# Kernel tuning notes

Measured on AMD Instinct MI355X. Metric: run time of the kernel, lower is better.

Reference implementation:

```python
import jax, jax.numpy as jnp
import numpy as np

WS = 8      # window_size
NH = 6      # num_heads
SHIFT = 4   # shift_size


def setup_inputs() -> dict:
    key = jax.random.key(0)
    k0, k1, k2, k3, k4 = jax.random.split(key, 5)
    B, C, H, W = 4, 192, 224, 224
    x = jax.random.normal(k0, (B, C, H, W), jnp.float32)
    # 1x1 convs == per-pixel linear layers: store weights as (out, in)
    w_qkv = jax.random.normal(k1, (3 * C, C), jnp.float32) * 0.05
    b_qkv = jax.random.normal(k2, (3 * C,), jnp.float32) * 0.05
    w_proj = jax.random.normal(k3, (C, C), jnp.float32) * 0.05
    b_proj = jax.random.normal(k4, (C,), jnp.float32) * 0.05
    return {"x": x, "w_qkv": w_qkv, "b_qkv": b_qkv, "w_proj": w_proj, "b_proj": b_proj}


def reference(x, w_qkv, b_qkv, w_proj, b_proj):
    B, C, H, W = x.shape
    hd = C // NH
    scale = hd ** -0.5

    if SHIFT > 0:
        x = jnp.roll(x, shift=(-SHIFT, -SHIFT), axis=(2, 3))

    pad_r = (WS - W % WS) % WS
    pad_b = (WS - H % WS) % WS
    if pad_r > 0 or pad_b > 0:
        x = jnp.pad(x, ((0, 0), (0, 0), (0, pad_b), (0, pad_r)))
    Hp, Wp = x.shape[2], x.shape[3]
    Hn, Wn = Hp // WS, Wp // WS

    # qkv 1x1 conv: (B,C,Hp,Wp) -> (B,3C,Hp,Wp)
    qkv = jnp.einsum('bchw,oc->bohw', x, w_qkv) + b_qkv[None, :, None, None]

    # (B,3,NH,hd,Hn,WS,Wn,WS) -> (3,B,Hn,Wn,NH,WS,WS,hd)
    qkv = qkv.reshape(B, 3, NH, hd, Hn, WS, Wn, WS)
    qkv = jnp.transpose(qkv, (1, 0, 4, 6, 2, 5, 7, 3))
    q = qkv[0].reshape(-1, NH, WS * WS, hd)  # (B*Hn*Wn, NH, 64, hd)
    k = qkv[1].reshape(-1, NH, WS * WS, hd)
    v = qkv[2].reshape(-1, NH, WS * WS, hd)

    attn = jax.nn.softmax(jnp.einsum('wnqd,wnkd->wnqk', q, k) * scale, axis=-1)
    out = jnp.einsum('wnqk,wnkd->wnqd', attn, v)

    # (B,Hn,Wn,NH,WS,WS,hd) -> (B,NH,hd,Hn,WS,Wn,WS) -> (B,C,Hp,Wp)
    out = out.reshape(B, Hn, Wn, NH, WS, WS, hd)
    out = jnp.transpose(out, (0, 3, 6, 1, 4, 2, 5)).reshape(B, C, Hp, Wp)

    out = jnp.einsum('bchw,oc->bohw', out, w_proj) + b_proj[None, :, None, None]

    if pad_r > 0 or pad_b > 0:
        out = out[:, :, :H, :W]
    if SHIFT > 0:
        out = jnp.roll(out, shift=(SHIFT, SHIFT), axis=(2, 3))
    return out
```

## Files before the change

### kernel.cpp

```cpp
#include <hip/hip_runtime.h>
#include <stdint.h>

#define HHW   224
#define CCH   192
#define SHIFT 4
#define NWIN  3136
#define NTOK  200704
#define QN    38535168ull

typedef __attribute__((ext_vector_type(8))) short bf16x8;
typedef __attribute__((ext_vector_type(4))) float f32x4;

__device__ __forceinline__ ushort f2bf(float f) {
    union { float f; uint32_t i; } v; v.f = f;
    uint32_t u = v.i;
    return (ushort)((u + 0x7FFFu + ((u >> 16) & 1u)) >> 16);
}
__device__ __forceinline__ uint32_t pk2(float a, float b) {
    return (uint32_t)f2bf(a) | ((uint32_t)f2bf(b) << 16);
}

__global__ __launch_bounds__(256) void prep_w(const float* __restrict__ w,
                                              ushort* __restrict__ wo, int nrow)
{
    int idx = blockIdx.x * 256 + threadIdx.x;
    if (idx >= nrow * 24) return;
    int rg = idx / 24, p = idx % 24;
    int s = p ^ (rg & 7);
    const float* src = w + (size_t)rg * 192 + s * 8;
    float4 a = *(const float4*)src;
    float4 b = *(const float4*)(src + 4);
    uint4 o;
    o.x = pk2(a.x, a.y); o.y = pk2(a.z, a.w);
    o.z = pk2(b.x, b.y); o.w = pk2(b.z, b.w);
    *(uint4*)(wo + (size_t)rg * 192 + p * 8) = o;
}

__global__ __launch_bounds__(256) void prep_x(const float* __restrict__ x,
                                              ushort* __restrict__ xo)
{
    __shared__ ushort lt[1792 * 8];
    const int blk = blockIdx.x;
    const int oct = blk % 24;
    const int bh  = blk / 24;
    const int hn  = bh % 28;
    const float* xb = x + ((size_t)(bh / 28) * CCH + oct * 8) * (HHW * HHW);

    for (int u = threadIdx.x; u < 448; u += 256) {
        int r = u / 56, q = u % 56;
        int hh = (hn * 8 + r + SHIFT) % HHW;
        int ww = (q * 4 + SHIFT) % HHW;
        const float* src = xb + (size_t)hh * HHW + ww;
        float4 v[8];
        #pragma unroll
        for (int c = 0; c < 8; c++)
            v[c] = *(const float4*)(src + (size_t)c * (HHW * HHW));
        #pragma unroll
        for (int i = 0; i < 4; i++) {
            int p = u * 4 + i;
            int sw = p ^ ((p >> 3) & 7);
            uint4 o;
            o.x = pk2(((const float*)&v[0])[i], ((const float*)&v[1])[i]);
            o.y = pk2(((const float*)&v[2])[i], ((const float*)&v[3])[i]);
            o.z = pk2(((const float*)&v[4])[i], ((const float*)&v[5])[i]);
            o.w = pk2(((const float*)&v[6])[i], ((const float*)&v[7])[i]);
            *(uint4*)&lt[sw * 8] = o;
        }
    }
    __syncthreads();

    for (int u = threadIdx.x; u < 1792; u += 256) {
        int wn = u >> 6, t = u & 63;
        int p = (t >> 3) * 224 + wn * 8 + (t & 7);
        int sw = p ^ ((p >> 3) & 7);
        *(uint4*)(xo + (size_t)(bh * 28 + wn) * 12288 + oct * 512 + t * 8) =
            *(const uint4*)&lt[sw * 8];
    }
}

template<int OCH>
__global__ __launch_bounds__(256, 3) void gemm_win(
    const ushort* __restrict__ xin, const ushort* __restrict__ wbf,
    const float* __restrict__ bias,
    ushort* __restrict__ qo, ushort* __restrict__ ko, ushort* __restrict__ vto,
    float* __restrict__ dout)
{
    __shared__ ushort wc[96 * 192];

    const int tid = threadIdx.x;
    const int wave = tid >> 6, lane = tid & 63;
    const int quad = lane >> 4, l16 = lane & 15;
    const int p0 = blockIdx.x * 128 + wave * 32;

    #pragma unroll
    for (int it = 0; it < 9; it++) {
        int off = (it * 4 + wave) * 512;
        __builtin_amdgcn_global_load_lds(
            (const __attribute__((address_space(1))) void*)(wbf + off + lane * 8),
            (__attribute__((address_space(3))) void*)(&wc[off]), 16, 0, 0);
    }

    bf16x8 bfr[2][6];
    #pragma unroll
    for (int nt = 0; nt < 2; nt++) {
        int token = p0 + nt * 16 + l16;
        #pragma unroll
        for (int k = 0; k < 6; k++) {
            if (OCH == 576)
                bfr[nt][k] = *(const bf16x8*)(xin + (size_t)(token >> 6) * 12288
                                              + (k * 4 + quad) * 512 + (token & 63) * 8);
            else
                bfr[nt][k] = *(const bf16x8*)(xin + (size_t)token * CCH + k * 32 + quad * 8);
        }
    }

    __syncthreads();

    #pragma unroll
    for (int ch = 0; ch < OCH / 96; ch++) {
        f32x4 acc[6][2];
        #pragma unroll
        for (int m = 0; m < 6; m++)
            #pragma unroll
            for (int nt = 0; nt < 2; nt++) acc[m][nt] = (f32x4){0.f, 0.f, 0.f, 0.f};

        const ushort* wl = wc + (size_t)l16 * 192;
        #pragma unroll
        for (int k = 0; k < 6; k++) {
            const ushort* wk = wl + ((k * 4 + quad) ^ (l16 & 7)) * 8;
            #pragma unroll
            for (int m = 0; m < 6; m++) {
                bf16x8 afrag = *(const bf16x8*)(wk + m * 3072);
                acc[m][0] = __builtin_amdgcn_mfma_f32_16x16x32_bf16(afrag, bfr[0][k], acc[m][0], 0, 0, 0);
                acc[m][1] = __builtin_amdgcn_mfma_f32_16x16x32_bf16(afrag, bfr[1][k], acc[m][1], 0, 0, 0);
            }
        }

        if (ch + 1 < OCH / 96) {
            __syncthreads();
            const ushort* wsrc = wbf + (size_t)(ch + 1) * (96 * 192);
            #pragma unroll
            for (int it = 0; it < 9; it++) {
                int off = (it * 4 + wave) * 512;
                __builtin_amdgcn_global_load_lds(
                    (const __attribute__((address_space(1))) void*)(wsrc + off + lane * 8),
                    (__attribute__((address_space(3))) void*)(&wc[off]), 16, 0, 0);
            }
        }

        const int obase = ch * 96;
        #pragma unroll
        for (int m = 0; m < 6; m++) {
            const int o0 = obase + m * 16 + quad * 4;
            float4 bb = *(const float4*)(bias + o0);
            #pragma unroll
            for (int nt = 0; nt < 2; nt++) {
                int token = p0 + nt * 16 + l16;
                int win = token >> 6, t = token & 63;
                float f0 = acc[m][nt][0] + bb.x, f1 = acc[m][nt][1] + bb.y;
                float f2 = acc[m][nt][2] + bb.z, f3 = acc[m][nt][3] + bb.w;
                if (OCH == 576) {
                    const int s = o0 / 192;
                    const int rem = o0 % 192;
                    const int h = rem >> 5, d0 = rem & 31;
                    size_t wh = (size_t)win * 6 + h;
                    if (s == 2) {
                        vto[(wh * 32 + d0 + 0) * 64 + t] = f2bf(f0);
                        vto[(wh * 32 + d0 + 1) * 64 + t] = f2bf(f1);
                        vto[(wh * 32 + d0 + 2) * 64 + t] = f2bf(f2);
                        vto[(wh * 32 + d0 + 3) * 64 + t] = f2bf(f3);
                    } else {
                        uint2 pk;
                        pk.x = pk2(f0, f1);
                        pk.y = pk2(f2, f3);
                        ushort* dst = (s == 0 ? qo : ko) + (wh * 64 + t) * 32 + d0;
                        *(uint2*)dst = pk;
                    }
                } else {
                    int b = win / 784, hn = (win / 28) % 28, wn = win % 28;
                    int hh = (hn * 8 + (t >> 3) + SHIFT) % HHW;
                    int ww = (wn * 8 + (t & 7) + SHIFT) % HHW;
                    float* dst = dout + ((size_t)(b * CCH + o0) * HHW + hh) * HHW + ww;
                    dst[0] = f0; dst[(size_t)HHW * HHW] = f1;
                    dst[2 * (size_t)HHW * HHW] = f2; dst[3 * (size_t)HHW * HHW] = f3;
                }
            }
        }
        if (ch + 1 < OCH / 96) __syncthreads();
    }
}

__global__ __launch_bounds__(384, 4) void attn_win(
    ushort* qx2,
    const ushort* __restrict__ k, const ushort* __restrict__ vt)
{
    __shared__ ushort pt[6][64 * 64];

    const int tid = threadIdx.x;
    const int h = tid >> 6, lane = tid & 63;
    const int quad = lane >> 4, l16 = lane & 15;
    const int win = blockIdx.x;

    const ushort* qp = qx2 + (size_t)(win * 6 + h) * 2048;
    const ushort* kp = k   + (size_t)(win * 6 + h) * 2048;
    const ushort* vp = vt  + (size_t)(win * 6 + h) * 2048;

    bf16x8 kf[4], qf[4], vf[2][2];
    #pragma unroll
    for (int nt = 0; nt < 4; nt++) kf[nt] = *(const bf16x8*)&kp[(nt * 16 + l16) * 32 + quad * 8];
    #pragma unroll
    for (int nt = 0; nt < 4; nt++) qf[nt] = *(const bf16x8*)&qp[(nt * 16 + l16) * 32 + quad * 8];
    #pragma unroll
    for (int md = 0; md < 2; md++)
        #pragma unroll
        for (int ks = 0; ks < 2; ks++)
            vf[md][ks] = *(const bf16x8*)&vp[(md * 16 + l16) * 64 + ks * 32 + quad * 8];

    const float SC = 0.25506953149031837f;
    ushort* ph = pt[h];

    #pragma unroll
    for (int nq = 0; nq < 4; nq += 2) {
        f32x4 sc[2][4];
        #pragma unroll
        for (int j = 0; j < 2; j++)
            #pragma unroll
            for (int mk = 0; mk < 4; mk++) {
                sc[j][mk] = (f32x4){0.f, 0.f, 0.f, 0.f};
                sc[j][mk] = __builtin_amdgcn_mfma_f32_16x16x32_bf16(kf[mk], qf[nq + j], sc[j][mk], 0, 0, 0);
            }
        #pragma unroll
        for (int j = 0; j < 2; j++) {
            float mx = sc[j][0][0];
            #pragma unroll
            for (int mk = 0; mk < 4; mk++)
                #pragma unroll
                for (int rg = 0; rg < 4; rg++) mx = fmaxf(mx, sc[j][mk][rg]);
            mx = fmaxf(mx, __shfl_xor(mx, 16, 64));
            mx = fmaxf(mx, __shfl_xor(mx, 32, 64));
            float e[4][4];
            float sm = 0.f;
            #pragma unroll
            for (int mk = 0; mk < 4; mk++)
                #pragma unroll
                for (int rg = 0; rg < 4; rg++) {
                    e[mk][rg] = exp2f((sc[j][mk][rg] - mx) * SC);
                    sm += e[mk][rg];
                }
            sm += __shfl_xor(sm, 16, 64);
            sm += __shfl_xor(sm, 32, 64);
            float r = __builtin_amdgcn_rcpf(sm);
            const int q = (nq + j) * 16 + l16;
            const int sx = q & 7;
            ushort* row = ph + q * 64;
            #pragma unroll
            for (int mk = 0; mk < 4; mk++) {
                uint2 w;
                w.x = pk2(e[mk][0] * r, e[mk][1] * r);
                w.y = pk2(e[mk][2] * r, e[mk][3] * r);
                int s0 = mk * 2 + (quad >> 1);
                *(uint2*)(row + (((s0 ^ sx) << 3) + (quad & 1) * 4)) = w;
            }
        }
    }
    __syncthreads();

    f32x4 o[2][4];
    #pragma unroll
    for (int md = 0; md < 2; md++)
        #pragma unroll
        for (int nq = 0; nq < 4; nq++) o[md][nq] = (f32x4){0.f, 0.f, 0.f, 0.f};
    #pragma unroll
    for (int ks = 0; ks < 2; ks++)
        #pragma unroll
        for (int nq = 0; nq < 4; nq++) {
            const int q = nq * 16 + l16;
            bf16x8 pf = *(const bf16x8*)(ph + q * 64 + ((((ks * 4 + quad) ^ (q & 7))) << 3));
            #pragma unroll
            for (int md = 0; md < 2; md++)
                o[md][nq] = __builtin_amdgcn_mfma_f32_16x16x32_bf16(vf[md][ks], pf, o[md][nq], 0, 0, 0);
        }

    ushort* x2 = qx2 + (size_t)win * 12288;
    #pragma unroll
    for (int md = 0; md < 2; md++)
        #pragma unroll
        for (int nq = 0; nq < 4; nq++) {
            const int q = nq * 16 + l16;
            const int c = h * 32 + md * 16 + quad * 4;
            uint2 w;
            w.x = pk2(o[md][nq][0], o[md][nq][1]);
            w.y = pk2(o[md][nq][2], o[md][nq][3]);
            *(uint2*)(x2 + q * CCH + c) = w;
        }
}

extern "C" void kernel_launch(void* const* d_in, const int* in_sizes, int n_in,
                              void* d_out, int out_size, void* d_ws, size_t ws_size,
                              hipStream_t stream) {
    const float* x      = (const float*)d_in[0];
    const float* w_qkv  = (const float*)d_in[1];
    const float* b_qkv  = (const float*)d_in[2];
    const float* w_proj = (const float*)d_in[3];
    const float* b_proj = (const float*)d_in[4];
    float* out = (float*)d_out;
    ushort* ws = (ushort*)d_ws;

    ushort* X1 = (ushort*)d_out;
    ushort* WQ = (ushort*)d_out + QN;
    ushort* Q  = ws;
    ushort* K  = ws + QN;
    ushort* VT = ws + 2 * QN;
    ushort* WP = VT;

    prep_w       <<<54, 256, 0, stream>>>(w_qkv, WQ, 576);
    prep_x       <<<4 * 28 * 24, 256, 0, stream>>>(x, X1);
    gemm_win<576><<<NTOK / 128, 256, 0, stream>>>(X1, WQ, b_qkv, Q, K, VT, nullptr);
    attn_win     <<<NWIN, 384, 0, stream>>>(Q, K, VT);
    prep_w       <<<18, 256, 0, stream>>>(w_proj, WP, 192);
    gemm_win<192><<<NTOK / 128, 256, 0, stream>>>(Q, WP, b_proj, nullptr, nullptr, nullptr, out);
}
```

Before: 514.2 us.

## Read GEMM weight fragments directly from global memory in MFMA-ready layout

New measurement: 670.4 us. 1.3x slower.

```diff
diff --git a/kernel.cpp b/kernel.cpp
--- a/kernel.cpp
+++ b/kernel.cpp
@@ -26,14 +26,17 @@
     int idx = blockIdx.x * 256 + threadIdx.x;
     if (idx >= nrow * 24) return;
     int rg = idx / 24, p = idx % 24;
-    int s = p ^ (rg & 7);
-    const float* src = w + (size_t)rg * 192 + s * 8;
+    int ch = rg / 96, mr = rg % 96;
+    int m = mr >> 4, l16 = mr & 15;
+    int k = p >> 2, quad = p & 3;
+    const float* src = w + (size_t)rg * 192 + p * 8;
     float4 a = *(const float4*)src;
     float4 b = *(const float4*)(src + 4);
     uint4 o;
     o.x = pk2(a.x, a.y); o.y = pk2(a.z, a.w);
     o.z = pk2(b.x, b.y); o.w = pk2(b.z, b.w);
-    *(uint4*)(wo + (size_t)rg * 192 + p * 8) = o;
+    size_t out = (size_t)((((ch * 6 + k) * 4 + quad) * 6 + m) * 16 + l16) * 8;
+    *(uint4*)(wo + out) = o;
 }
 
 __global__ __launch_bounds__(256) void prep_x(const float* __restrict__ x,
@@ -79,26 +82,16 @@
 }
 
 template<int OCH>
-__global__ __launch_bounds__(256, 3) void gemm_win(
+__global__ __launch_bounds__(256, 2) void gemm_win(
     const ushort* __restrict__ xin, const ushort* __restrict__ wbf,
     const float* __restrict__ bias,
     ushort* __restrict__ qo, ushort* __restrict__ ko, ushort* __restrict__ vto,
     float* __restrict__ dout)
 {
-    __shared__ ushort wc[96 * 192];
-
     const int tid = threadIdx.x;
     const int wave = tid >> 6, lane = tid & 63;
     const int quad = lane >> 4, l16 = lane & 15;
     const int p0 = blockIdx.x * 128 + wave * 32;
-
-    #pragma unroll
-    for (int it = 0; it < 9; it++) {
-        int off = (it * 4 + wave) * 512;
-        __builtin_amdgcn_global_load_lds(
-            (const __attribute__((address_space(1))) void*)(wbf + off + lane * 8),
-            (__attribute__((address_space(3))) void*)(&wc[off]), 16, 0, 0);
-    }
 
     bf16x8 bfr[2][6];
     #pragma unroll
@@ -114,37 +107,24 @@
         }
     }
 
-    __syncthreads();
-
     #pragma unroll
     for (int ch = 0; ch < OCH / 96; ch++) {
+        const ushort* wch = wbf + (size_t)ch * (96 * 192);
+
         f32x4 acc[6][2];
         #pragma unroll
         for (int m = 0; m < 6; m++)
             #pragma unroll
             for (int nt = 0; nt < 2; nt++) acc[m][nt] = (f32x4){0.f, 0.f, 0.f, 0.f};
 
-        const ushort* wl = wc + (size_t)l16 * 192;
         #pragma unroll
         for (int k = 0; k < 6; k++) {
-            const ushort* wk = wl + ((k * 4 + quad) ^ (l16 & 7)) * 8;
+            const ushort* wk = wch + ((k * 4 + quad) * 96 + l16) * 8;
             #pragma unroll
             for (int m = 0; m < 6; m++) {
-                bf16x8 afrag = *(const bf16x8*)(wk + m * 3072);
+                bf16x8 afrag = *(const bf16x8*)(wk + m * 128);
                 acc[m][0] = __builtin_amdgcn_mfma_f32_16x16x32_bf16(afrag, bfr[0][k], acc[m][0], 0, 0, 0);
                 acc[m][1] = __builtin_amdgcn_mfma_f32_16x16x32_bf16(afrag, bfr[1][k], acc[m][1], 0, 0, 0);
-            }
-        }
-
-        if (ch + 1 < OCH / 96) {
-            __syncthreads();
-            const ushort* wsrc = wbf + (size_t)(ch + 1) * (96 * 192);
-            #pragma unroll
-            for (int it = 0; it < 9; it++) {
-                int off = (it * 4 + wave) * 512;
-                __builtin_amdgcn_global_load_lds(
-                    (const __attribute__((address_space(1))) void*)(wsrc + off + lane * 8),
-                    (__attribute__((address_space(3))) void*)(&wc[off]), 16, 0, 0);
             }
         }
 
@@ -186,7 +166,6 @@
                 }
             }
         }
-        if (ch + 1 < OCH / 96) __syncthreads();
     }
 }
 
```

## Fuse QKV projection into window attention kernel, keeping Q/K/V in LDS

Applied to the files above, without the earlier changes.

After: 506.9 us. No clear change (-1.4%).

```diff
diff --git a/kernel.cpp b/kernel.cpp
--- a/kernel.cpp
+++ b/kernel.cpp
@@ -26,14 +26,17 @@
     int idx = blockIdx.x * 256 + threadIdx.x;
     if (idx >= nrow * 24) return;
     int rg = idx / 24, p = idx % 24;
-    int s = p ^ (rg & 7);
-    const float* src = w + (size_t)rg * 192 + s * 8;
+    int ch = rg / 96, mr = rg % 96;
+    int m = mr >> 4, l16 = mr & 15;
+    int k = p >> 2, quad = p & 3;
+    const float* src = w + (size_t)rg * 192 + p * 8;
     float4 a = *(const float4*)src;
     float4 b = *(const float4*)(src + 4);
     uint4 o;
     o.x = pk2(a.x, a.y); o.y = pk2(a.z, a.w);
     o.z = pk2(b.x, b.y); o.w = pk2(b.z, b.w);
-    *(uint4*)(wo + (size_t)rg * 192 + p * 8) = o;
+    size_t out = (size_t)((((ch * 6 + k) * 4 + quad) * 6 + m) * 16 + l16) * 8;
+    *(uint4*)(wo + out) = o;
 }
 
 __global__ __launch_bounds__(256) void prep_x(const float* __restrict__ x,
@@ -78,146 +81,106 @@
     }
 }
 
-template<int OCH>
-__global__ __launch_bounds__(256, 3) void gemm_win(
-    const ushort* __restrict__ xin, const ushort* __restrict__ wbf,
+__global__ __launch_bounds__(384, 1) void qkv_attn_win(
+    const ushort* __restrict__ xin,
+    const ushort* __restrict__ wbf,
     const float* __restrict__ bias,
-    ushort* __restrict__ qo, ushort* __restrict__ ko, ushort* __restrict__ vto,
-    float* __restrict__ dout)
+    ushort* __restrict__ x2o)
 {
-    __shared__ ushort wc[96 * 192];
+    __shared__ char smem[162816];
+    char* qb = smem + 73728;
+    char* kb = smem + 104448;
+    char* vb = smem + 135168;
 
     const int tid = threadIdx.x;
-    const int wave = tid >> 6, lane = tid & 63;
+    const int wave = tid / 64, lane = tid & 63;
     const int quad = lane >> 4, l16 = lane & 15;
-    const int p0 = blockIdx.x * 128 + wave * 32;
-
-    #pragma unroll
-    for (int it = 0; it < 9; it++) {
-        int off = (it * 4 + wave) * 512;
+    const int win = blockIdx.x;
+
+    bf16x8 bfr[4][6];
+    const ushort* xw = xin + (size_t)win * 12288;
+    #pragma unroll
+    for (int nt = 0; nt < 4; nt++)
+        #pragma unroll
+        for (int k = 0; k < 6; k++)
+            bfr[nt][k] = *(const bf16x8*)(xw + (k * 4 + quad) * 512 + (nt * 16 + l16) * 8);
+
+    #pragma unroll
+    for (int it = 0; it < 6; it++) {
+        int off = it * 3072 + wave * 512;
         __builtin_amdgcn_global_load_lds(
             (const __attribute__((address_space(1))) void*)(wbf + off + lane * 8),
-            (__attribute__((address_space(3))) void*)(&wc[off]), 16, 0, 0);
-    }
-
-    bf16x8 bfr[2][6];
-    #pragma unroll
-    for (int nt = 0; nt < 2; nt++) {
-        int token = p0 + nt * 16 + l16;
-        #pragma unroll
-        for (int k = 0; k < 6; k++) {
-            if (OCH == 576)
-                bfr[nt][k] = *(const bf16x8*)(xin + (size_t)(token >> 6) * 12288
-                                              + (k * 4 + quad) * 512 + (token & 63) * 8);
-            else
-                bfr[nt][k] = *(const bf16x8*)(xin + (size_t)token * CCH + k * 32 + quad * 8);
-        }
-    }
-
+            (__attribute__((address_space(3))) void*)(smem + off * 2), 16, 0, 0);
+    }
     __syncthreads();
 
     #pragma unroll
-    for (int ch = 0; ch < OCH / 96; ch++) {
-        f32x4 acc[6][2];
-        #pragma unroll
-        for (int m = 0; m < 6; m++)
-            #pragma unroll
-            for (int nt = 0; nt < 2; nt++) acc[m][nt] = (f32x4){0.f, 0.f, 0.f, 0.f};
-
-        const ushort* wl = wc + (size_t)l16 * 192;
-        #pragma unroll
-        for (int k = 0; k < 6; k++) {
-            const ushort* wk = wl + ((k * 4 + quad) ^ (l16 & 7)) * 8;
-            #pragma unroll
-            for (int m = 0; m < 6; m++) {
-                bf16x8 afrag = *(const bf16x8*)(wk + m * 3072);
-                acc[m][0] = __builtin_amdgcn_mfma_f32_16x16x32_bf16(afrag, bfr[0][k], acc[m][0], 0, 0, 0);
-                acc[m][1] = __builtin_amdgcn_mfma_f32_16x16x32_bf16(afrag, bfr[1][k], acc[m][1], 0, 0, 0);
-            }
-        }
-
-        if (ch + 1 < OCH / 96) {
-            __syncthreads();
-            const ushort* wsrc = wbf + (size_t)(ch + 1) * (96 * 192);
-            #pragma unroll
-            for (int it = 0; it < 9; it++) {
-                int off = (it * 4 + wave) * 512;
+    for (int ch = 0; ch < 6; ch++) {
+        if (ch < 5) {
+            const ushort* wsrc = wbf + (size_t)(ch + 1) * 18432;
+            char* dbuf = smem + ((ch + 1) & 1) * 36864;
+            #pragma unroll
+            for (int it = 0; it < 6; it++) {
+                int off = it * 3072 + wave * 512;
                 __builtin_amdgcn_global_load_lds(
                     (const __attribute__((address_space(1))) void*)(wsrc + off + lane * 8),
-                    (__attribute__((address_space(3))) void*)(&wc[off]), 16, 0, 0);
-            }
-        }
-
-        const int obase = ch * 96;
-        #pragma unroll
-        for (int m = 0; m < 6; m++) {
-            const int o0 = obase + m * 16 + quad * 4;
-            float4 bb = *(const float4*)(bias + o0);
-            #pragma unroll
-            for (int nt = 0; nt < 2; nt++) {
-                int token = p0 + nt * 16 + l16;
-                int win = token >> 6, t = token & 63;
-                float f0 = acc[m][nt][0] + bb.x, f1 = acc[m][nt][1] + bb.y;
-                float f2 = acc[m][nt][2] + bb.z, f3 = acc[m][nt][3] + bb.w;
-                if (OCH == 576) {
-                    const int s = o0 / 192;
-                    const int rem = o0 % 192;
-                    const int h = rem >> 5, d0 = rem & 31;
-                    size_t wh = (size_t)win * 6 + h;
-                    if (s == 2) {
-                        vto[(wh * 32 + d0 + 0) * 64 + t] = f2bf(f0);
-                        vto[(wh * 32 + d0 + 1) * 64 + t] = f2bf(f1);
-                        vto[(wh * 32 + d0 + 2) * 64 + t] = f2bf(f2);
-                        vto[(wh * 32 + d0 + 3) * 64 + t] = f2bf(f3);
-                    } else {
-                        uint2 pk;
-                        pk.x = pk2(f0, f1);
-                        pk.y = pk2(f2, f3);
-                        ushort* dst = (s == 0 ? qo : ko) + (wh * 64 + t) * 32 + d0;
-                        *(uint2*)dst = pk;
-                    }
-                } else {
-                    int b = win / 784, hn = (win / 28) % 28, wn = win % 28;
-                    int hh = (hn * 8 + (t >> 3) + SHIFT) % HHW;
-                    int ww = (wn * 8 + (t & 7) + SHIFT) % HHW;
-                    float* dst = dout + ((size_t)(b * CCH + o0) * HHW + hh) * HHW + ww;
-                    dst[0] = f0; dst[(size_t)HHW * HHW] = f1;
-                    dst[2 * (size_t)HHW * HHW] = f2; dst[3 * (size_t)HHW * HHW] = f3;
-                }
-            }
-        }
-        if (ch + 1 < OCH / 96) __syncthreads();
-    }
-}
-
-__global__ __launch_bounds__(384, 4) void attn_win(
-    ushort* qx2,
-    const ushort* __restrict__ k, const ushort* __restrict__ vt)
-{
-    __shared__ ushort pt[6][64 * 64];
-
-    const int tid = threadIdx.x;
-    const int h = tid >> 6, lane = tid & 63;
-    const int quad = lane >> 4, l16 = lane & 15;
-    const int win = blockIdx.x;
-
-    const ushort* qp = qx2 + (size_t)(win * 6 + h) * 2048;
-    const ushort* kp = k   + (size_t)(win * 6 + h) * 2048;
-    const ushort* vp = vt  + (size_t)(win * 6 + h) * 2048;
-
+                    (__attribute__((address_space(3))) void*)(dbuf + off * 2), 16, 0, 0);
+            }
+        }
+        const ushort* cur = (const ushort*)(smem + (ch & 1) * 36864);
+
+        f32x4 acc[4];
+        #pragma unroll
+        for (int nt = 0; nt < 4; nt++) acc[nt] = (f32x4){0.f, 0.f, 0.f, 0.f};
+        #pragma unroll
+        for (int k = 0; k < 6; k++) {
+            bf16x8 af = *(const bf16x8*)(cur + ((k * 4 + quad) * 96 + wave * 16 + l16) * 8);
+            #pragma unroll
+            for (int nt = 0; nt < 4; nt++)
+                acc[nt] = __builtin_amdgcn_mfma_f32_16x16x32_bf16(af, bfr[nt][k], acc[nt], 0, 0, 0);
+        }
+
+        const int o0c = ch * 96 + wave * 16 + quad * 4;
+        float4 bb = *(const float4*)(bias + o0c);
+        const int rem = (ch & 1) * 96 + wave * 16 + quad * 4;
+        const int h = rem >> 5, d0 = rem & 31;
+        #pragma unroll
+        for (int nt = 0; nt < 4; nt++) {
+            const int t = nt * 16 + l16;
+            float f0 = acc[nt][0] + bb.x, f1 = acc[nt][1] + bb.y;
+            float f2 = acc[nt][2] + bb.z, f3 = acc[nt][3] + bb.w;
+            if (ch < 4) {
+                char* base = (ch < 2 ? qb : kb);
+                uint2 w;
+                w.x = pk2(f0, f1); w.y = pk2(f2, f3);
+                *(uint2*)(base + h * 5120 + t * 80 + d0 * 2) = w;
+            } else {
+                ushort* vh = (ushort*)(vb + h * 4608);
+                vh[(d0 + 0) * 72 + t] = f2bf(f0);
+                vh[(d0 + 1) * 72 + t] = f2bf(f1);
+                vh[(d0 + 2) * 72 + t] = f2bf(f2);
+                vh[(d0 + 3) * 72 + t] = f2bf(f3);
+            }
+        }
+        __syncthreads();
+    }
+
+    const int h = wave;
     bf16x8 kf[4], qf[4], vf[2][2];
     #pragma unroll
-    for (int nt = 0; nt < 4; nt++) kf[nt] = *(const bf16x8*)&kp[(nt * 16 + l16) * 32 + quad * 8];
-    #pragma unroll
-    for (int nt = 0; nt < 4; nt++) qf[nt] = *(const bf16x8*)&qp[(nt * 16 + l16) * 32 + quad * 8];
+    for (int nt = 0; nt < 4; nt++)
+        qf[nt] = *(const bf16x8*)(qb + h * 5120 + (nt * 16 + l16) * 80 + quad * 16);
+    #pragma unroll
+    for (int nt = 0; nt < 4; nt++)
+        kf[nt] = *(const bf16x8*)(kb + h * 5120 + (nt * 16 + l16) * 80 + quad * 16);
     #pragma unroll
     for (int md = 0; md < 2; md++)
         #pragma unroll
         for (int ks = 0; ks < 2; ks++)
-            vf[md][ks] = *(const bf16x8*)&vp[(md * 16 + l16) * 64 + ks * 32 + quad * 8];
+            vf[md][ks] = *(const bf16x8*)(vb + h * 4608 + (md * 16 + l16) * 144 + ks * 64 + quad * 16);
 
     const float SC = 0.25506953149031837f;
-    ushort* ph = pt[h];
+    ushort* ph = (ushort*)smem + h * 4096;
 
     #pragma unroll
     for (int nq = 0; nq < 4; nq += 2) {
@@ -263,7 +226,6 @@
             }
         }
     }
-    __syncthreads();
 
     f32x4 o[2][4];
     #pragma unroll
@@ -281,7 +243,7 @@
                 o[md][nq] = __builtin_amdgcn_mfma_f32_16x16x32_bf16(vf[md][ks], pf, o[md][nq], 0, 0, 0);
         }
 
-    ushort* x2 = qx2 + (size_t)win * 12288;
+    ushort* x2 = x2o + (size_t)win * 12288;
     #pragma unroll
     for (int md = 0; md < 2; md++)
         #pragma unroll
@@ -293,6 +255,89 @@
             w.y = pk2(o[md][nq][2], o[md][nq][3]);
             *(uint2*)(x2 + q * CCH + c) = w;
         }
+}
+
+__global__ __launch_bounds__(256, 3) void gemm_proj(
+    const ushort* __restrict__ xin, const ushort* __restrict__ wbf,
+    const float* __restrict__ bias, float* __restrict__ dout)
+{
+    __shared__ ushort wc[96 * 192];
+
+    const int tid = threadIdx.x;
+    const int wave = tid >> 6, lane = tid & 63;
+    const int quad = lane >> 4, l16 = lane & 15;
+    const int p0 = blockIdx.x * 128 + wave * 32;
+
+    #pragma unroll
+    for (int it = 0; it < 9; it++) {
+        int off = (it * 4 + wave) * 512;
+        __builtin_amdgcn_global_load_lds(
+            (const __attribute__((address_space(1))) void*)(wbf + off + lane * 8),
+            (__attribute__((address_space(3))) void*)(&wc[off]), 16, 0, 0);
+    }
+
+    bf16x8 bfr[2][6];
+    #pragma unroll
+    for (int nt = 0; nt < 2; nt++) {
+        int token = p0 + nt * 16 + l16;
+        #pragma unroll
+        for (int k = 0; k < 6; k++)
+            bfr[nt][k] = *(const bf16x8*)(xin + (size_t)token * CCH + k * 32 + quad * 8);
+    }
+
+    __syncthreads();
+
+    #pragma unroll
+    for (int ch = 0; ch < 2; ch++) {
+        f32x4 acc[6][2];
+        #pragma unroll
+        for (int m = 0; m < 6; m++)
+            #pragma unroll
+            for (int nt = 0; nt < 2; nt++) acc[m][nt] = (f32x4){0.f, 0.f, 0.f, 0.f};
+
+        #pragma unroll
+        for (int k = 0; k < 6; k++) {
+            #pragma unroll
+            for (int m = 0; m < 6; m++) {
+                bf16x8 afrag = *(const bf16x8*)(wc + ((k * 4 + quad) * 96 + m * 16 + l16) * 8);
+                acc[m][0] = __builtin_amdgcn_mfma_f32_16x16x32_bf16(afrag, bfr[0][k], acc[m][0], 0, 0, 0);
+                acc[m][1] = __builtin_amdgcn_mfma_f32_16x16x32_bf16(afrag, bfr[1][k], acc[m][1], 0, 0, 0);
+            }
+        }
+
+        if (ch + 1 < 2) {
+            __syncthreads();
+            const ushort* wsrc = wbf + (size_t)18432;
+            #pragma unroll
+            for (int it = 0; it < 9; it++) {
+                int off = (it * 4 + wave) * 512;
+                __builtin_amdgcn_global_load_lds(
+                    (const __attribute__((address_space(1))) void*)(wsrc + off + lane * 8),
+                    (__attribute__((address_space(3))) void*)(&wc[off]), 16, 0, 0);
+            }
+        }
+
+        const int obase = ch * 96;
+        #pragma unroll
+        for (int m = 0; m < 6; m++) {
+            const int o0 = obase + m * 16 + quad * 4;
+            float4 bb = *(const float4*)(bias + o0);
+            #pragma unroll
+            for (int nt = 0; nt < 2; nt++) {
+                int token = p0 + nt * 16 + l16;
+                int win = token >> 6, t = token & 63;
+                float f0 = acc[m][nt][0] + bb.x, f1 = acc[m][nt][1] + bb.y;
+                float f2 = acc[m][nt][2] + bb.z, f3 = acc[m][nt][3] + bb.w;
+                int b = win / 784, hn = (win / 28) % 28, wn = win % 28;
+                int hh = (hn * 8 + (t >> 3) + SHIFT) % HHW;
+                int ww = (wn * 8 + (t & 7) + SHIFT) % HHW;
+                float* dst = dout + ((size_t)(b * CCH + o0) * HHW + hh) * HHW + ww;
+                dst[0] = f0; dst[(size_t)HHW * HHW] = f1;
+                dst[2 * (size_t)HHW * HHW] = f2; dst[3 * (size_t)HHW * HHW] = f3;
+            }
+        }
+        if (ch + 1 < 2) __syncthreads();
+    }
 }
 
 extern "C" void kernel_launch(void* const* d_in, const int* in_sizes, int n_in,
@@ -308,15 +353,12 @@
 
     ushort* X1 = (ushort*)d_out;
     ushort* WQ = (ushort*)d_out + QN;
-    ushort* Q  = ws;
-    ushort* K  = ws + QN;
-    ushort* VT = ws + 2 * QN;
-    ushort* WP = VT;
-
-    prep_w       <<<54, 256, 0, stream>>>(w_qkv, WQ, 576);
-    prep_x       <<<4 * 28 * 24, 256, 0, stream>>>(x, X1);
-    gemm_win<576><<<NTOK / 128, 256, 0, stream>>>(X1, WQ, b_qkv, Q, K, VT, nullptr);
-    attn_win     <<<NWIN, 384, 0, stream>>>(Q, K, VT);
-    prep_w       <<<18, 256, 0, stream>>>(w_proj, WP, 192);
-    gemm_win<192><<<NTOK / 128, 256, 0, stream>>>(Q, WP, b_proj, nullptr, nullptr, nullptr, out);
-}
+    ushort* X2 = ws;
+    ushort* WP = ws + QN;
+
+    prep_w      <<<54, 256, 0, stream>>>(w_qkv, WQ, 576);
+    prep_x      <<<4 * 28 * 24, 256, 0, stream>>>(x, X1);
+    qkv_attn_win<<<NWIN, 384, 0, stream>>>(X1, WQ, b_qkv, X2);
+    prep_w      <<<18, 256, 0, stream>>>(w_proj, WP, 192);
+    gemm_proj   <<<NTOK / 128, 256, 0, stream>>>(X2, WP, b_proj, out);
+}
```
